# Optimization experiments

Measured on AMD Instinct MI355X. Metric: run time of the kernel, lower is better.

## Reference

```python
import jax, jax.numpy as jnp
import numpy as np

B, C, H, W = 4, 64, 128, 128
K = 3
KK = K * K
EPS = 1e-5


def setup_inputs() -> dict:
    key = jax.random.key(0)
    ks = jax.random.split(key, 8)
    s = 0.05
    return {
        "x": jax.random.normal(ks[0], (B, C, H, W), jnp.float32),
        "dw_w": jax.random.normal(ks[1], (C, 1, K, K), jnp.float32) * s,
        "dw_b": jax.random.normal(ks[2], (C,), jnp.float32) * s,
        "bn_gamma": jnp.ones((C,), jnp.float32),
        "bn_beta": jnp.zeros((C,), jnp.float32),
        "pw_w": jax.random.normal(ks[3], (2 * KK, C), jnp.float32) * s,
        "pw_b": jax.random.normal(ks[4], (2 * KK,), jnp.float32) * s,
        "skip_scale": jnp.ones((1,), jnp.float32),
        "deform_w": jax.random.normal(ks[5], (C, C, K, K), jnp.float32) * s,
        "deform_b": jax.random.normal(ks[6], (C,), jnp.float32) * s,
    }


def _bilinear_sample(x, py, px):
    # x: [B,C,H,W]; py,px: [B,KK,H,W] float sample coords. Zero padding outside.
    b, c, h, w = x.shape
    y0 = jnp.floor(py)
    x0 = jnp.floor(px)
    wy = py - y0
    wx = px - x0
    y0i = y0.astype(jnp.int32)
    x0i = x0.astype(jnp.int32)
    x_flat = x.reshape(b, c, h * w)

    def gather(yi, xi):
        valid = (yi >= 0) & (yi < h) & (xi >= 0) & (xi < w)
        yc = jnp.clip(yi, 0, h - 1)
        xc = jnp.clip(xi, 0, w - 1)
        idx = (yc * w + xc).reshape(b, -1)  # [B, KK*H*W]
        v = jax.vmap(lambda xb, ib: xb[:, ib])(x_flat, idx)  # [B,C,KK*H*W]
        v = v.reshape(b, c, *yi.shape[1:])  # [B,C,KK,H,W]
        return v * valid[:, None].astype(x.dtype)

    v00 = gather(y0i, x0i)
    v01 = gather(y0i, x0i + 1)
    v10 = gather(y0i + 1, x0i)
    v11 = gather(y0i + 1, x0i + 1)
    wy = wy[:, None]  # [B,1,KK,H,W]
    wx = wx[:, None]
    return (v00 * (1 - wy) * (1 - wx) + v01 * (1 - wy) * wx
            + v10 * wy * (1 - wx) + v11 * wy * wx)


def reference(x, dw_w, dw_b, bn_gamma, bn_beta, pw_w, pw_b, skip_scale, deform_w, deform_b):
    b, c, h, w = x.shape
    # depthwise conv (padding='same') + bias
    dw = jax.lax.conv_general_dilated(
        x, dw_w, window_strides=(1, 1), padding='SAME',
        feature_group_count=c, dimension_numbers=('NCHW', 'OIHW', 'NCHW')
    ) + dw_b[None, :, None, None]
    # BatchNorm2d, training-mode batch statistics
    mean = jnp.mean(dw, axis=(0, 2, 3))
    var = jnp.var(dw, axis=(0, 2, 3))
    x_dw = ((dw - mean[None, :, None, None]) * jax.lax.rsqrt(var + EPS)[None, :, None, None]
            * bn_gamma[None, :, None, None] + bn_beta[None, :, None, None])
    # pointwise conv -> offsets [B, 2*KK, H, W], (dy, dx) pairs per kernel tap
    off = jnp.einsum('oc,bchw->bohw', pw_w, x_dw) + pw_b[None, :, None, None]
    off = off.reshape(b, KK, 2, h, w)
    ky, kx = jnp.meshgrid(jnp.arange(K), jnp.arange(K), indexing='ij')
    # sample coords: out pixel - pad + kernel tap + offset
    py = (jnp.arange(h, dtype=x.dtype)[None, None, :, None] - 1.0
          + ky.reshape(KK).astype(x.dtype)[None, :, None, None] + off[:, :, 0])
    px = (jnp.arange(w, dtype=x.dtype)[None, None, None, :] - 1.0
          + kx.reshape(KK).astype(x.dtype)[None, :, None, None] + off[:, :, 1])
    sampled = _bilinear_sample(x, py, px)  # [B,C,KK,H,W]
    x_deform = (jnp.einsum('bckhw,ock->bohw', sampled, deform_w.reshape(deform_w.shape[0], c, KK))
                + deform_b[None, :, None, None])
    return x_deform + x_dw + x * skip_scale
```

## Files before the change

kernel.cpp:

```cpp
#include <hip/hip_runtime.h>

#define Bn 4
#define Cn 64
#define Hn 128
#define Wn 128
#define HWn (Hn*Wn)
#define NPIX (Bn*HWn)
#define KKn 9
#define NOFF 18
#define EPSf 1e-5f

#define OFF_DWT   0u
#define OFF_XTH   4194304u
#define OFF_GEOM  6291456u
#define OFF_WT    7471104u
#define OFF_SSUM  7507968u
#define OFF_SSQ   7508032u

typedef __attribute__((ext_vector_type(8))) short short8v;
typedef __attribute__((ext_vector_type(8))) unsigned short ushort8v;
typedef __attribute__((ext_vector_type(4))) float float4v;

__device__ __forceinline__ unsigned short f2bf(float f) {
  unsigned u = __builtin_bit_cast(unsigned, f);
  u += 0x7fffu + ((u >> 16) & 1u);
  return (unsigned short)(u >> 16);
}
__device__ __forceinline__ float b2f(unsigned short u) {
  return __builtin_bit_cast(float, ((unsigned)u) << 16);
}

#define MKADDR(GG, B00, B01, B10, B11, M00, M01, M10, M11)                    \
  {                                                                           \
    float py_ = (GG).x, px_ = (GG).y;                                         \
    float y0f_ = floorf(py_), x0f_ = floorf(px_);                             \
    float wy_ = py_ - y0f_, wx_ = px_ - x0f_;                                 \
    int y0_ = (int)y0f_, x0_ = (int)x0f_;                                     \
    int y1_ = y0_ + 1, x1_ = x0_ + 1;                                         \
    bool vy0_ = (y0_ >= 0) && (y0_ < Hn), vy1_ = (y1_ >= 0) && (y1_ < Hn);    \
    bool vx0_ = (x0_ >= 0) && (x0_ < Wn), vx1_ = (x1_ >= 0) && (x1_ < Wn);    \
    int y0c_ = vy0_ ? y0_ : 0, y1c_ = vy1_ ? y1_ : 0;                         \
    int x0c_ = vx0_ ? x0_ : 0, x1c_ = vx1_ ? x1_ : 0;                         \
    M00 = (vy0_ && vx0_) ? (1.f - wy_) * (1.f - wx_) : 0.f;                   \
    M01 = (vy0_ && vx1_) ? (1.f - wy_) * wx_ : 0.f;                           \
    M10 = (vy1_ && vx0_) ? wy_ * (1.f - wx_) : 0.f;                           \
    M11 = (vy1_ && vx1_) ? wy_ * wx_ : 0.f;                                   \
    B00 = xb + (size_t)((y0c_ * Wn + x0c_) * 64);                             \
    B01 = xb + (size_t)((y0c_ * Wn + x1c_) * 64);                             \
    B10 = xb + (size_t)((y1c_ * Wn + x0c_) * 64);                             \
    B11 = xb + (size_t)((y1c_ * Wn + x1c_) * 64);                             \
  }

__global__ __launch_bounds__(256) void k1_dw_t4(
    const float* __restrict__ x, const float* __restrict__ dw_w,
    const float* __restrict__ dw_b, unsigned short* __restrict__ XTH,
    float* __restrict__ DWT, float* __restrict__ ssum, float* __restrict__ ssq)
{
  __shared__ float lds_dw[64][65];
  __shared__ float lds_xt[64][65];
  const int t = threadIdx.x;
  const int pxl = t & 63;
  const int cg = t >> 6;
  const int p = blockIdx.x * 64 + pxl;
  const int b = p >> 14; const int sp = p & 16383;
  const int h = sp >> 7; const int w = sp & 127;

  int so[9]; float mval[9];
  #pragma unroll
  for (int tt = 0; tt < 9; tt++) {
    int dy = tt / 3 - 1, dx = tt % 3 - 1;
    int hh = h + dy, ww = w + dx;
    bool v = (hh >= 0) && (hh < Hn) && (ww >= 0) && (ww < Wn);
    int hc = v ? hh : h; int wc = v ? ww : w;
    so[tt] = hc * Wn + wc;
    mval[tt] = v ? 1.f : 0.f;
  }
  const float* xb = x + (size_t)b * Cn * HWn;

  #pragma unroll
  for (int j = 0; j < 16; j++) {
    int c = cg * 16 + j;
    const float* xc = xb + (size_t)c * HWn;
    float acc = dw_b[c];
    #pragma unroll
    for (int tt = 0; tt < 9; tt++)
      acc += (mval[tt] * xc[so[tt]]) * dw_w[c * 9 + tt];
    lds_dw[pxl][c] = acc;
    lds_xt[pxl][c] = xc[sp];
  }
  __syncthreads();

  #pragma unroll
  for (int k = 0; k < 4; k++) {
    int px_l = k * 16 + (t >> 4);
    int c_l  = (t & 15) * 4;
    float4 v = *(float4*)&lds_dw[px_l][c_l];
    size_t pp = (size_t)blockIdx.x * 64 + px_l;
    *(float4*)&DWT[pp * 64 + c_l] = v;
  }
  #pragma unroll
  for (int k = 0; k < 2; k++) {
    int px_l = k * 32 + (t >> 3);
    int cg8  = (t & 7) * 8;
    unsigned pk[4];
    #pragma unroll
    for (int j = 0; j < 4; j++) {
      unsigned short lo = f2bf(lds_xt[px_l][cg8 + 2 * j]);
      unsigned short hi = f2bf(lds_xt[px_l][cg8 + 2 * j + 1]);
      pk[j] = (unsigned)lo | ((unsigned)hi << 16);
    }
    size_t pp = (size_t)blockIdx.x * 64 + px_l;
    *(uint4*)&XTH[pp * 64 + cg8] = make_uint4(pk[0], pk[1], pk[2], pk[3]);
  }

  int cc = t & 63, grp = t >> 6;
  float s = 0.f, q = 0.f;
  #pragma unroll
  for (int i = 0; i < 16; i++) {
    float v = lds_dw[grp * 16 + i][cc];
    s += v; q += v * v;
  }
  __syncthreads();
  float* scratch = &lds_xt[0][0];
  scratch[t] = s; scratch[256 + t] = q;
  __syncthreads();
  if (t < 64) {
    float s0 = scratch[t] + scratch[t + 64] + scratch[t + 128] + scratch[t + 192];
    float q0 = scratch[256 + t] + scratch[256 + t + 64] +
               scratch[256 + t + 128] + scratch[256 + t + 192];
    atomicAdd(&ssum[t], s0);
    atomicAdd(&ssq[t], q0);
  }
}

__global__ __launch_bounds__(256) void k_wt(const float* __restrict__ dwf,
                                            unsigned short* __restrict__ WT2)
{
  int t = blockIdx.x * 256 + threadIdx.x;
  if (t >= 64 * 64 * 9) return;
  int c = t & 63; int o = (t >> 6) & 63; int kk = t >> 12;
  WT2[t] = f2bf(dwf[(o * 64 + c) * 9 + kk]);
}

__global__ __launch_bounds__(256) void k3_offsets2(const float* __restrict__ DWT,
    const float* __restrict__ ssum, const float* __restrict__ ssq,
    const float* __restrict__ gamma, const float* __restrict__ beta,
    const float* __restrict__ pw_w, const float* __restrict__ pw_b,
    float* __restrict__ GEOM2)
{
  __shared__ float s_sc[64], s_sh[64];
  int t = threadIdx.x;
  if (t < 64) {
    float n = (float)NPIX;
    float mean = ssum[t] / n;
    float var = ssq[t] / n - mean * mean;
    float sc = gamma[t] * rsqrtf(var + EPSf);
    s_sc[t] = sc;
    s_sh[t] = beta[t] - mean * sc;
  }
  __syncthreads();

  int p = blockIdx.x * 256 + t;
  int sp = p & 16383; int h = sp >> 7; int w = sp & 127;
  float off[NOFF];
  #pragma unroll
  for (int o = 0; o < NOFF; o++) off[o] = pw_b[o];
  const float4* dp = (const float4*)(DWT + (size_t)p * 64);
  #pragma unroll
  for (int c4 = 0; c4 < 16; c4++) {
    float4 d = dp[c4];
    int c = c4 * 4;
    float x0 = d.x * s_sc[c]     + s_sh[c];
    float x1 = d.y * s_sc[c + 1] + s_sh[c + 1];
    float x2 = d.z * s_sc[c + 2] + s_sh[c + 2];
    float x3 = d.w * s_sc[c + 3] + s_sh[c + 3];
    #pragma unroll
    for (int o = 0; o < NOFF; o++) {
      const float* pw = pw_w + o * 64 + c;
      off[o] += pw[0] * x0 + pw[1] * x1 + pw[2] * x2 + pw[3] * x3;
    }
  }
  #pragma unroll
  for (int kk = 0; kk < KKn; kk++) {
    float py = (float)h - 1.f + (float)(kk / 3) + off[2 * kk];
    float px = (float)w - 1.f + (float)(kk % 3) + off[2 * kk + 1];
    float2* g = (float2*)(GEOM2 + ((size_t)kk * NPIX + p) * 2);
    *g = make_float2(py, px);
  }
}

__global__ __launch_bounds__(256) void k4_mfma5(
    const unsigned short* __restrict__ XTH, const float* __restrict__ DWT,
    const float* __restrict__ GEOM2, const unsigned short* __restrict__ WT2,
    const float* __restrict__ ssum, const float* __restrict__ ssq,
    const float* __restrict__ gamma, const float* __restrict__ beta,
    const float* __restrict__ deform_b, const float* __restrict__ skip_scale,
    float* __restrict__ out)
{
  __shared__ float s_sc[64], s_sh[64];
  const int tid = threadIdx.x;
  if (tid < 64) {
    float n = (float)NPIX;
    float mean = ssum[tid] / n;
    float var = ssq[tid] / n - mean * mean;
    float sc = gamma[tid] * rsqrtf(var + EPSf);
    s_sc[tid] = sc;
    s_sh[tid] = beta[tid] - mean * sc;
  }
  __syncthreads();

  const int lane = tid & 63;
  const int wv = tid >> 6;
  const int l15 = lane & 15;
  const int lg = lane >> 4;
  const int bid = blockIdx.x;
  const int swz = (bid & 7) * 128 + (bid >> 3);
  const int p0 = swz * 64;
  const int b = p0 >> 14;
  const int pw0 = p0 + wv * 16;
  const int c8 = lg * 8;

  float4v acc0 = {0.f,0.f,0.f,0.f}, acc1 = {0.f,0.f,0.f,0.f};
  float4v acc2 = {0.f,0.f,0.f,0.f}, acc3 = {0.f,0.f,0.f,0.f};

  const unsigned short* xb = XTH + (size_t)b * HWn * 64;

  float2 g_n = *(const float2*)(GEOM2 + ((size_t)0 * NPIX + pw0 + l15) * 2);
  float cm00, cm01, cm10, cm11, nm00, nm01, nm10, nm11;
  const unsigned short *pb00, *pb01, *pb10, *pb11;
  ushort8v c0a,c0b,c0c,c0d, c1a,c1b,c1c,c1d;
  ushort8v n0a,n0b,n0c,n0d, n1a,n1b,n1c,n1d;

  MKADDR(g_n, pb00, pb01, pb10, pb11, cm00, cm01, cm10, cm11);
  c0a = *(const ushort8v*)(pb00 + c8);      c0b = *(const ushort8v*)(pb01 + c8);
  c0c = *(const ushort8v*)(pb10 + c8);      c0d = *(const ushort8v*)(pb11 + c8);
  c1a = *(const ushort8v*)(pb00 + 32 + c8); c1b = *(const ushort8v*)(pb01 + 32 + c8);
  c1c = *(const ushort8v*)(pb10 + 32 + c8); c1d = *(const ushort8v*)(pb11 + 32 + c8);
  g_n = *(const float2*)(GEOM2 + ((size_t)1 * NPIX + pw0 + l15) * 2);

  #pragma unroll
  for (int kk = 0; kk < KKn; kk++) {
    if (kk < 8) {
      MKADDR(g_n, pb00, pb01, pb10, pb11, nm00, nm01, nm10, nm11);
      n0a = *(const ushort8v*)(pb00 + c8);      n0b = *(const ushort8v*)(pb01 + c8);
      n0c = *(const ushort8v*)(pb10 + c8);      n0d = *(const ushort8v*)(pb11 + c8);
      n1a = *(const ushort8v*)(pb00 + 32 + c8); n1b = *(const ushort8v*)(pb01 + 32 + c8);
      n1c = *(const ushort8v*)(pb10 + 32 + c8); n1d = *(const ushort8v*)(pb11 + 32 + c8);
    }
    short8v af0, af1;
    #pragma unroll
    for (int j = 0; j < 8; j++) {
      float s0 = b2f(c0a[j]) * cm00 + b2f(c0b[j]) * cm01 +
                 b2f(c0c[j]) * cm10 + b2f(c0d[j]) * cm11;
      af0[j] = (short)f2bf(s0);
      float s1 = b2f(c1a[j]) * cm00 + b2f(c1b[j]) * cm01 +
                 b2f(c1c[j]) * cm10 + b2f(c1d[j]) * cm11;
      af1[j] = (short)f2bf(s1);
    }
    const unsigned short* wtkk = WT2 + (size_t)kk * 4096 + (size_t)l15 * 64 + c8;
    {
      short8v ba = *(const short8v*)(wtkk);
      short8v bb = *(const short8v*)(wtkk + 32);
      acc0 = __builtin_amdgcn_mfma_f32_16x16x32_bf16(af0, ba, acc0, 0, 0, 0);
      acc0 = __builtin_amdgcn_mfma_f32_16x16x32_bf16(af1, bb, acc0, 0, 0, 0);
    }
    {
      short8v ba = *(const short8v*)(wtkk + 16 * 64);
      short8v bb = *(const short8v*)(wtkk + 16 * 64 + 32);
      acc1 = __builtin_amdgcn_mfma_f32_16x16x32_bf16(af0, ba, acc1, 0, 0, 0);
      acc1 = __builtin_amdgcn_mfma_f32_16x16x32_bf16(af1, bb, acc1, 0, 0, 0);
    }
    {
      short8v ba = *(const short8v*)(wtkk + 32 * 64);
      short8v bb = *(const short8v*)(wtkk + 32 * 64 + 32);
      acc2 = __builtin_amdgcn_mfma_f32_16x16x32_bf16(af0, ba, acc2, 0, 0, 0);
      acc2 = __builtin_amdgcn_mfma_f32_16x16x32_bf16(af1, bb, acc2, 0, 0, 0);
    }
    {
      short8v ba = *(const short8v*)(wtkk + 48 * 64);
      short8v bb = *(const short8v*)(wtkk + 48 * 64 + 32);
      acc3 = __builtin_amdgcn_mfma_f32_16x16x32_bf16(af0, ba, acc3, 0, 0, 0);
      acc3 = __builtin_amdgcn_mfma_f32_16x16x32_bf16(af1, bb, acc3, 0, 0, 0);
    }
    if (kk < 8) {
      cm00 = nm00; cm01 = nm01; cm10 = nm10; cm11 = nm11;
      c0a = n0a; c0b = n0b; c0c = n0c; c0d = n0d;
      c1a = n1a; c1b = n1b; c1c = n1c; c1d = n1d;
      if (kk < 7)
        g_n = *(const float2*)(GEOM2 + ((size_t)(kk + 2) * NPIX + pw0 + l15) * 2);
    }
  }

  float sk = skip_scale[0];
  #pragma unroll
  for (int nt = 0; nt < 4; nt++) {
    int o = nt * 16 + l15;
    float sc = s_sc[o], sh = s_sh[o], db = deform_b[o];
    float* outb = out + ((size_t)(b * 64 + o)) * HWn;
    float4v a = (nt == 0) ? acc0 : (nt == 1) ? acc1 : (nt == 2) ? acc2 : acc3;
    #pragma unroll
    for (int r = 0; r < 4; r++) {
      int p = pw0 + lg * 4 + r;
      int sp = p & 16383;
      float dv = DWT[(size_t)p * 64 + o];
      float xv = b2f(XTH[(size_t)p * 64 + o]);
      outb[sp] = a[r] + db + dv * sc + sh + xv * sk;
    }
  }
}

extern "C" void kernel_launch(void* const* d_in, const int* in_sizes, int n_in,
                              void* d_out, int out_size, void* d_ws, size_t ws_size,
                              hipStream_t stream)
{
  const float* x        = (const float*)d_in[0];
  const float* dw_w     = (const float*)d_in[1];
  const float* dw_b     = (const float*)d_in[2];
  const float* bn_gamma = (const float*)d_in[3];
  const float* bn_beta  = (const float*)d_in[4];
  const float* pw_w     = (const float*)d_in[5];
  const float* pw_b     = (const float*)d_in[6];
  const float* skip     = (const float*)d_in[7];
  const float* deform_w = (const float*)d_in[8];
  const float* deform_b = (const float*)d_in[9];
  float* out = (float*)d_out;
  float* ws  = (float*)d_ws;

  unsigned short* XTH = (unsigned short*)(ws + OFF_XTH);
  unsigned short* WT2 = (unsigned short*)(ws + OFF_WT);

  hipMemsetAsync(ws + OFF_SSUM, 0, 2 * 64 * sizeof(float), stream);

  k_wt<<<144, 256, 0, stream>>>(deform_w, WT2);
  k1_dw_t4<<<1024, 256, 0, stream>>>(x, dw_w, dw_b, XTH, ws + OFF_DWT,
                                     ws + OFF_SSUM, ws + OFF_SSQ);
  k3_offsets2<<<256, 256, 0, stream>>>(ws + OFF_DWT, ws + OFF_SSUM, ws + OFF_SSQ,
                                       bn_gamma, bn_beta, pw_w, pw_b, ws + OFF_GEOM);
  k4_mfma5<<<1024, 256, 0, stream>>>(XTH, ws + OFF_DWT, ws + OFF_GEOM, WT2,
                                     ws + OFF_SSUM, ws + OFF_SSQ, bn_gamma, bn_beta,
                                     deform_b, skip, out);
}
```

Measured before the change: 217.6 us.

## Split deform kernel taps across waves and halve per-block work in prep kernels

The deform MFMA kernel now has two waves cooperate on one 16-pixel tile. Each wave handles part of the 9 kernel taps, and the partial accumulators are exchanged through LDS before a split epilogue. This replaces the single-wave explicit double-buffered prefetch. The depthwise kernel processes 32 pixels per block instead of 64, and the offsets kernel splits the channel reduction across two half-blocks combined via LDS. All three changes raise the number of blocks and waves in flight to hide gather latency, at the cost of extra LDS traffic, a sync, and losing the explicit prefetch pipeline.

After: 235.6 us. 8.3% more time.

```diff
diff --git a/kernel.cpp b/kernel.cpp
--- a/kernel.cpp
+++ b/kernel.cpp
@@ -51,17 +51,17 @@
     B11 = xb + (size_t)((y1c_ * Wn + x1c_) * 64);                             \
   }
 
-__global__ __launch_bounds__(256) void k1_dw_t4(
+__global__ __launch_bounds__(256) void k1_dw_t5(
     const float* __restrict__ x, const float* __restrict__ dw_w,
     const float* __restrict__ dw_b, unsigned short* __restrict__ XTH,
     float* __restrict__ DWT, float* __restrict__ ssum, float* __restrict__ ssq)
 {
-  __shared__ float lds_dw[64][65];
-  __shared__ float lds_xt[64][65];
+  __shared__ float lds_dw[32][65];
+  __shared__ float lds_xt[32][65];
   const int t = threadIdx.x;
-  const int pxl = t & 63;
-  const int cg = t >> 6;
-  const int p = blockIdx.x * 64 + pxl;
+  const int pxl = t & 31;
+  const int cg = t >> 5;
+  const int p = blockIdx.x * 32 + pxl;
   const int b = p >> 14; const int sp = p & 16383;
   const int h = sp >> 7; const int w = sp & 127;
 
@@ -78,8 +78,8 @@
   const float* xb = x + (size_t)b * Cn * HWn;
 
   #pragma unroll
-  for (int j = 0; j < 16; j++) {
-    int c = cg * 16 + j;
+  for (int j = 0; j < 8; j++) {
+    int c = cg * 8 + j;
     const float* xc = xb + (size_t)c * HWn;
     float acc = dw_b[c];
     #pragma unroll
@@ -91,16 +91,15 @@
   __syncthreads();
 
   #pragma unroll
-  for (int k = 0; k < 4; k++) {
+  for (int k = 0; k < 2; k++) {
     int px_l = k * 16 + (t >> 4);
     int c_l  = (t & 15) * 4;
     float4 v = *(float4*)&lds_dw[px_l][c_l];
-    size_t pp = (size_t)blockIdx.x * 64 + px_l;
+    size_t pp = (size_t)blockIdx.x * 32 + px_l;
     *(float4*)&DWT[pp * 64 + c_l] = v;
   }
-  #pragma unroll
-  for (int k = 0; k < 2; k++) {
-    int px_l = k * 32 + (t >> 3);
+  {
+    int px_l = t >> 3;
     int cg8  = (t & 7) * 8;
     unsigned pk[4];
     #pragma unroll
@@ -109,15 +108,15 @@
       unsigned short hi = f2bf(lds_xt[px_l][cg8 + 2 * j + 1]);
       pk[j] = (unsigned)lo | ((unsigned)hi << 16);
     }
-    size_t pp = (size_t)blockIdx.x * 64 + px_l;
+    size_t pp = (size_t)blockIdx.x * 32 + px_l;
     *(uint4*)&XTH[pp * 64 + cg8] = make_uint4(pk[0], pk[1], pk[2], pk[3]);
   }
 
   int cc = t & 63, grp = t >> 6;
   float s = 0.f, q = 0.f;
   #pragma unroll
-  for (int i = 0; i < 16; i++) {
-    float v = lds_dw[grp * 16 + i][cc];
+  for (int i = 0; i < 8; i++) {
+    float v = lds_dw[grp * 8 + i][cc];
     s += v; q += v * v;
   }
   __syncthreads();
@@ -142,13 +141,14 @@
   WT2[t] = f2bf(dwf[(o * 64 + c) * 9 + kk]);
 }
 
-__global__ __launch_bounds__(256) void k3_offsets2(const float* __restrict__ DWT,
+__global__ __launch_bounds__(256) void k3_offsets3(const float* __restrict__ DWT,
     const float* __restrict__ ssum, const float* __restrict__ ssq,
     const float* __restrict__ gamma, const float* __restrict__ beta,
     const float* __restrict__ pw_w, const float* __restrict__ pw_b,
     float* __restrict__ GEOM2)
 {
   __shared__ float s_sc[64], s_sh[64];
+  __shared__ float s_par[128][NOFF + 1];
   int t = threadIdx.x;
   if (t < 64) {
     float n = (float)NPIX;
@@ -160,14 +160,16 @@
   }
   __syncthreads();
 
-  int p = blockIdx.x * 256 + t;
+  int pxl = t & 127; int hf = t >> 7;
+  int p = blockIdx.x * 128 + pxl;
   int sp = p & 16383; int h = sp >> 7; int w = sp & 127;
   float off[NOFF];
   #pragma unroll
-  for (int o = 0; o < NOFF; o++) off[o] = pw_b[o];
+  for (int o = 0; o < NOFF; o++) off[o] = hf ? 0.f : pw_b[o];
   const float4* dp = (const float4*)(DWT + (size_t)p * 64);
   #pragma unroll
-  for (int c4 = 0; c4 < 16; c4++) {
+  for (int c4i = 0; c4i < 8; c4i++) {
+    int c4 = hf * 8 + c4i;
     float4 d = dp[c4];
     int c = c4 * 4;
     float x0 = d.x * s_sc[c]     + s_sh[c];
@@ -180,16 +182,85 @@
       off[o] += pw[0] * x0 + pw[1] * x1 + pw[2] * x2 + pw[3] * x3;
     }
   }
-  #pragma unroll
-  for (int kk = 0; kk < KKn; kk++) {
-    float py = (float)h - 1.f + (float)(kk / 3) + off[2 * kk];
-    float px = (float)w - 1.f + (float)(kk % 3) + off[2 * kk + 1];
-    float2* g = (float2*)(GEOM2 + ((size_t)kk * NPIX + p) * 2);
-    *g = make_float2(py, px);
-  }
-}
-
-__global__ __launch_bounds__(256) void k4_mfma5(
+  if (hf == 1) {
+    #pragma unroll
+    for (int o = 0; o < NOFF; o++) s_par[pxl][o] = off[o];
+  }
+  __syncthreads();
+  if (hf == 0) {
+    #pragma unroll
+    for (int o = 0; o < NOFF; o++) off[o] += s_par[pxl][o];
+    #pragma unroll
+    for (int kk = 0; kk < KKn; kk++) {
+      float py = (float)h - 1.f + (float)(kk / 3) + off[2 * kk];
+      float px = (float)w - 1.f + (float)(kk % 3) + off[2 * kk + 1];
+      float2* g = (float2*)(GEOM2 + ((size_t)kk * NPIX + p) * 2);
+      *g = make_float2(py, px);
+    }
+  }
+}
+
+template<int KB, int KE>
+__device__ __forceinline__ void kloop(
+    const unsigned short* __restrict__ xb, const float* __restrict__ GEOM2,
+    const unsigned short* __restrict__ WT2, int pw0, int l15, int c8,
+    float4v& acc0, float4v& acc1, float4v& acc2, float4v& acc3)
+{
+  float2 g = *(const float2*)(GEOM2 + ((size_t)KB * NPIX + pw0 + l15) * 2);
+  #pragma unroll
+  for (int kk = KB; kk < KE; kk++) {
+    float m00, m01, m10, m11;
+    const unsigned short *pb00, *pb01, *pb10, *pb11;
+    MKADDR(g, pb00, pb01, pb10, pb11, m00, m01, m10, m11);
+    if (kk + 1 < KE)
+      g = *(const float2*)(GEOM2 + ((size_t)(kk + 1) * NPIX + pw0 + l15) * 2);
+    ushort8v u0a = *(const ushort8v*)(pb00 + c8);
+    ushort8v u0b = *(const ushort8v*)(pb01 + c8);
+    ushort8v u0c = *(const ushort8v*)(pb10 + c8);
+    ushort8v u0d = *(const ushort8v*)(pb11 + c8);
+    ushort8v u1a = *(const ushort8v*)(pb00 + 32 + c8);
+    ushort8v u1b = *(const ushort8v*)(pb01 + 32 + c8);
+    ushort8v u1c = *(const ushort8v*)(pb10 + 32 + c8);
+    ushort8v u1d = *(const ushort8v*)(pb11 + 32 + c8);
+    short8v af0, af1;
+    #pragma unroll
+    for (int j = 0; j < 8; j++) {
+      float s0 = b2f(u0a[j]) * m00 + b2f(u0b[j]) * m01 +
+                 b2f(u0c[j]) * m10 + b2f(u0d[j]) * m11;
+      af0[j] = (short)f2bf(s0);
+      float s1 = b2f(u1a[j]) * m00 + b2f(u1b[j]) * m01 +
+                 b2f(u1c[j]) * m10 + b2f(u1d[j]) * m11;
+      af1[j] = (short)f2bf(s1);
+    }
+    const unsigned short* wtkk = WT2 + (size_t)kk * 4096 + (size_t)l15 * 64 + c8;
+    {
+      short8v ba = *(const short8v*)(wtkk);
+      short8v bb = *(const short8v*)(wtkk + 32);
+      acc0 = __builtin_amdgcn_mfma_f32_16x16x32_bf16(af0, ba, acc0, 0, 0, 0);
+      acc0 = __builtin_amdgcn_mfma_f32_16x16x32_bf16(af1, bb, acc0, 0, 0, 0);
+    }
+    {
+      short8v ba = *(const short8v*)(wtkk + 16 * 64);
+      short8v bb = *(const short8v*)(wtkk + 16 * 64 + 32);
+      acc1 = __builtin_amdgcn_mfma_f32_16x16x32_bf16(af0, ba, acc1, 0, 0, 0);
+      acc1 = __builtin_amdgcn_mfma_f32_16x16x32_bf16(af1, bb, acc1, 0, 0, 0);
+    }
+    {
+      short8v ba = *(const short8v*)(wtkk + 32 * 64);
+      short8v bb = *(const short8v*)(wtkk + 32 * 64 + 32);
+      acc2 = __builtin_amdgcn_mfma_f32_16x16x32_bf16(af0, ba, acc2, 0, 0, 0);
+      acc2 = __builtin_amdgcn_mfma_f32_16x16x32_bf16(af1, bb, acc2, 0, 0, 0);
+    }
+    {
+      short8v ba = *(const short8v*)(wtkk + 48 * 64);
+      short8v bb = *(const short8v*)(wtkk + 48 * 64 + 32);
+      acc3 = __builtin_amdgcn_mfma_f32_16x16x32_bf16(af0, ba, acc3, 0, 0, 0);
+      acc3 = __builtin_amdgcn_mfma_f32_16x16x32_bf16(af1, bb, acc3, 0, 0, 0);
+    }
+  }
+}
+
+__global__ __launch_bounds__(128) void k4_mfma7(
     const unsigned short* __restrict__ XTH, const float* __restrict__ DWT,
     const float* __restrict__ GEOM2, const unsigned short* __restrict__ WT2,
     const float* __restrict__ ssum, const float* __restrict__ ssq,
@@ -198,6 +269,7 @@
     float* __restrict__ out)
 {
   __shared__ float s_sc[64], s_sh[64];
+  __shared__ float s_xch[2][64][9];
   const int tid = threadIdx.x;
   if (tid < 64) {
     float n = (float)NPIX;
@@ -214,99 +286,60 @@
   const int l15 = lane & 15;
   const int lg = lane >> 4;
   const int bid = blockIdx.x;
-  const int swz = (bid & 7) * 128 + (bid >> 3);
-  const int p0 = swz * 64;
-  const int b = p0 >> 14;
-  const int pw0 = p0 + wv * 16;
-  const int c8 = lg * 8;
+  const int swz = (bid & 7) * 512 + (bid >> 3);
+  const int pw0 = swz * 16;
+  const int b = pw0 >> 14;
 
   float4v acc0 = {0.f,0.f,0.f,0.f}, acc1 = {0.f,0.f,0.f,0.f};
   float4v acc2 = {0.f,0.f,0.f,0.f}, acc3 = {0.f,0.f,0.f,0.f};
 
   const unsigned short* xb = XTH + (size_t)b * HWn * 64;
-
-  float2 g_n = *(const float2*)(GEOM2 + ((size_t)0 * NPIX + pw0 + l15) * 2);
-  float cm00, cm01, cm10, cm11, nm00, nm01, nm10, nm11;
-  const unsigned short *pb00, *pb01, *pb10, *pb11;
-  ushort8v c0a,c0b,c0c,c0d, c1a,c1b,c1c,c1d;
-  ushort8v n0a,n0b,n0c,n0d, n1a,n1b,n1c,n1d;
-
-  MKADDR(g_n, pb00, pb01, pb10, pb11, cm00, cm01, cm10, cm11);
-  c0a = *(const ushort8v*)(pb00 + c8);      c0b = *(const ushort8v*)(pb01 + c8);
-  c0c = *(const ushort8v*)(pb10 + c8);      c0d = *(const ushort8v*)(pb11 + c8);
-  c1a = *(const ushort8v*)(pb00 + 32 + c8); c1b = *(const ushort8v*)(pb01 + 32 + c8);
-  c1c = *(const ushort8v*)(pb10 + 32 + c8); c1d = *(const ushort8v*)(pb11 + 32 + c8);
-  g_n = *(const float2*)(GEOM2 + ((size_t)1 * NPIX + pw0 + l15) * 2);
-
-  #pragma unroll
-  for (int kk = 0; kk < KKn; kk++) {
-    if (kk < 8) {
-      MKADDR(g_n, pb00, pb01, pb10, pb11, nm00, nm01, nm10, nm11);
-      n0a = *(const ushort8v*)(pb00 + c8);      n0b = *(const ushort8v*)(pb01 + c8);
-      n0c = *(const ushort8v*)(pb10 + c8);      n0d = *(const ushort8v*)(pb11 + c8);
-      n1a = *(const ushort8v*)(pb00 + 32 + c8); n1b = *(const ushort8v*)(pb01 + 32 + c8);
-      n1c = *(const ushort8v*)(pb10 + 32 + c8); n1d = *(const ushort8v*)(pb11 + 32 + c8);
-    }
-    short8v af0, af1;
-    #pragma unroll
-    for (int j = 0; j < 8; j++) {
-      float s0 = b2f(c0a[j]) * cm00 + b2f(c0b[j]) * cm01 +
-                 b2f(c0c[j]) * cm10 + b2f(c0d[j]) * cm11;
-      af0[j] = (short)f2bf(s0);
-      float s1 = b2f(c1a[j]) * cm00 + b2f(c1b[j]) * cm01 +
-                 b2f(c1c[j]) * cm10 + b2f(c1d[j]) * cm11;
-      af1[j] = (short)f2bf(s1);
-    }
-    const unsigned short* wtkk = WT2 + (size_t)kk * 4096 + (size_t)l15 * 64 + c8;
-    {
-      short8v ba = *(const short8v*)(wtkk);
-      short8v bb = *(const short8v*)(wtkk + 32);
-      acc0 = __builtin_amdgcn_mfma_f32_16x16x32_bf16(af0, ba, acc0, 0, 0, 0);
-      acc0 = __builtin_amdgcn_mfma_f32_16x16x32_bf16(af1, bb, acc0, 0, 0, 0);
-    }
-    {
-      short8v ba = *(const short8v*)(wtkk + 16 * 64);
-      short8v bb = *(const short8v*)(wtkk + 16 * 64 + 32);
-      acc1 = __builtin_amdgcn_mfma_f32_16x16x32_bf16(af0, ba, acc1, 0, 0, 0);
-      acc1 = __builtin_amdgcn_mfma_f32_16x16x32_bf16(af1, bb, acc1, 0, 0, 0);
-    }
-    {
-      short8v ba = *(const short8v*)(wtkk + 32 * 64);
-      short8v bb = *(const short8v*)(wtkk + 32 * 64 + 32);
-      acc2 = __builtin_amdgcn_mfma_f32_16x16x32_bf16(af0, ba, acc2, 0, 0, 0);
-      acc2 = __builtin_amdgcn_mfma_f32_16x16x32_bf16(af1, bb, acc2, 0, 0, 0);
-    }
-    {
-      short8v ba = *(const short8v*)(wtkk + 48 * 64);
-      short8v bb = *(const short8v*)(wtkk + 48 * 64 + 32);
-      acc3 = __builtin_amdgcn_mfma_f32_16x16x32_bf16(af0, ba, acc3, 0, 0, 0);
-      acc3 = __builtin_amdgcn_mfma_f32_16x16x32_bf16(af1, bb, acc3, 0, 0, 0);
-    }
-    if (kk < 8) {
-      cm00 = nm00; cm01 = nm01; cm10 = nm10; cm11 = nm11;
-      c0a = n0a; c0b = n0b; c0c = n0c; c0d = n0d;
-      c1a = n1a; c1b = n1b; c1c = n1c; c1d = n1d;
-      if (kk < 7)
-        g_n = *(const float2*)(GEOM2 + ((size_t)(kk + 2) * NPIX + pw0 + l15) * 2);
-    }
-  }
+  const int c8 = lg * 8;
+
+  if (wv == 0)
+    kloop<0, 5>(xb, GEOM2, WT2, pw0, l15, c8, acc0, acc1, acc2, acc3);
+  else
+    kloop<5, 9>(xb, GEOM2, WT2, pw0, l15, c8, acc0, acc1, acc2, acc3);
+
+  if (wv == 0) {
+    #pragma unroll
+    for (int r = 0; r < 4; r++) {
+      s_xch[0][lane][r] = acc2[r]; s_xch[0][lane][4 + r] = acc3[r];
+    }
+  } else {
+    #pragma unroll
+    for (int r = 0; r < 4; r++) {
+      s_xch[1][lane][r] = acc0[r]; s_xch[1][lane][4 + r] = acc1[r];
+    }
+  }
+  __syncthreads();
 
   float sk = skip_scale[0];
-  #pragma unroll
-  for (int nt = 0; nt < 4; nt++) {
-    int o = nt * 16 + l15;
-    float sc = s_sc[o], sh = s_sh[o], db = deform_b[o];
-    float* outb = out + ((size_t)(b * 64 + o)) * HWn;
-    float4v a = (nt == 0) ? acc0 : (nt == 1) ? acc1 : (nt == 2) ? acc2 : acc3;
+#define EPI(NT, A)                                                            \
+  { int o = (NT) * 16 + l15;                                                  \
+    float sc_ = s_sc[o], sh_ = s_sh[o], db_ = deform_b[o];                    \
+    float* outb = out + ((size_t)(b * 64 + o)) * HWn;                         \
+    _Pragma("unroll")                                                         \
+    for (int r = 0; r < 4; r++) {                                             \
+      int pp = pw0 + lg * 4 + r; int sp = pp & 16383;                         \
+      float dv = DWT[(size_t)pp * 64 + o];                                    \
+      float xv = b2f(XTH[(size_t)pp * 64 + o]);                               \
+      outb[sp] = A[r] + db_ + dv * sc_ + sh_ + xv * sk; } }
+
+  if (wv == 0) {
     #pragma unroll
     for (int r = 0; r < 4; r++) {
-      int p = pw0 + lg * 4 + r;
-      int sp = p & 16383;
-      float dv = DWT[(size_t)p * 64 + o];
-      float xv = b2f(XTH[(size_t)p * 64 + o]);
-      outb[sp] = a[r] + db + dv * sc + sh + xv * sk;
-    }
-  }
+      acc0[r] += s_xch[1][lane][r]; acc1[r] += s_xch[1][lane][4 + r];
+    }
+    EPI(0, acc0); EPI(1, acc1);
+  } else {
+    #pragma unroll
+    for (int r = 0; r < 4; r++) {
+      acc2[r] += s_xch[0][lane][r]; acc3[r] += s_xch[0][lane][4 + r];
+    }
+    EPI(2, acc2); EPI(3, acc3);
+  }
+#undef EPI
 }
 
 extern "C" void kernel_launch(void* const* d_in, const int* in_sizes, int n_in,
@@ -332,11 +365,11 @@
   hipMemsetAsync(ws + OFF_SSUM, 0, 2 * 64 * sizeof(float), stream);
 
   k_wt<<<144, 256, 0, stream>>>(deform_w, WT2);
-  k1_dw_t4<<<1024, 256, 0, stream>>>(x, dw_w, dw_b, XTH, ws + OFF_DWT,
+  k1_dw_t5<<<2048, 256, 0, stream>>>(x, dw_w, dw_b, XTH, ws + OFF_DWT,
                                      ws + OFF_SSUM, ws + OFF_SSQ);
-  k3_offsets2<<<256, 256, 0, stream>>>(ws + OFF_DWT, ws + OFF_SSUM, ws + OFF_SSQ,
+  k3_offsets3<<<512, 256, 0, stream>>>(ws + OFF_DWT, ws + OFF_SSUM, ws + OFF_SSQ,
                                        bn_gamma, bn_beta, pw_w, pw_b, ws + OFF_GEOM);
-  k4_mfma5<<<1024, 256, 0, stream>>>(XTH, ws + OFF_DWT, ws + OFF_GEOM, WT2,
+  k4_mfma7<<<4096, 128, 0, stream>>>(XTH, ws + OFF_DWT, ws + OFF_GEOM, WT2,
                                      ws + OFF_SSUM, ws + OFF_SSQ, bn_gamma, bn_beta,
                                      deform_b, skip, out);
 }
```
